# Optimization experiments

Measured on AMD Instinct MI355X. Metric: run time of the kernel, lower is better.

Reference implementation:

```python
import jax, jax.numpy as jnp
import numpy as np
import math

L, Bt, IN, H = 512, 128, 512, 60


def setup_inputs() -> dict:
    key = jax.random.key(0)
    k1, k2, k3 = jax.random.split(key, 3)
    inp = jax.random.normal(k1, (L, Bt, IN), dtype=jnp.float32)
    W = jax.random.normal(k2, (H, IN), dtype=jnp.float32) / np.sqrt(IN)
    b = jnp.zeros((H,), dtype=jnp.float32)
    alphabet = jax.random.uniform(k3, (H, 3), dtype=jnp.float32, minval=-math.pi, maxval=math.pi)
    bond_lengths = jnp.array([132.868, 145.801, 152.326], dtype=jnp.float32)
    bond_angles = jnp.array([2.028, 2.124, 1.941], dtype=jnp.float32)
    return {"inp": inp, "W": W, "b": b, "alphabet": alphabet,
            "bond_lengths": bond_lengths, "bond_angles": bond_angles}


def reference(inp, W, b, alphabet, bond_lengths, bond_angles):
    Lr, Bb = inp.shape[0], inp.shape[1]
    # mixture over alphabet of torsion angles
    x = jax.nn.softmax(inp @ W.T + b, axis=2)                 # (L, B, H)
    phi = jnp.arctan2(x @ jnp.sin(alphabet), x @ jnp.cos(alphabet))  # (L, B, 3)
    # per residue i the loop consumes phi[i].T -> bond index is fastest axis
    phi_f = phi.transpose(0, 2, 1).reshape(Lr * 3, Bb)        # (3L, B)
    r = jnp.tile(bond_lengths, Lr)[:, None]                   # (3L, 1)
    th = jnp.tile(bond_angles, Lr)[:, None]                   # (3L, 1)
    # SRF coordinates of every new atom
    c_tilde = jnp.stack([
        (r * jnp.cos(th)) * jnp.ones_like(phi_f),
        r * jnp.cos(phi_f) * jnp.sin(th),
        r * jnp.sin(phi_f) * jnp.sin(th),
    ], axis=-1)                                               # (3L, B, 3)

    e = jnp.eye(3, dtype=inp.dtype)
    carry0 = (jnp.broadcast_to(e[0], (Bb, 3)),
              jnp.broadcast_to(e[1], (Bb, 3)),
              jnp.broadcast_to(e[2], (Bb, 3)))

    def step(carry, ct):
        A, Bp, C = carry                                      # each (B, 3)
        BC = C - Bp
        bc = BC / jnp.linalg.norm(BC, axis=1, keepdims=True)
        AB = Bp - A
        Nv = jnp.cross(AB, bc)
        n = Nv / jnp.linalg.norm(Nv, axis=1, keepdims=True)
        # D = C + R @ c_tilde, R columns = [bc, n x bc, n]
        D = C + bc * ct[:, 0:1] + jnp.cross(n, bc) * ct[:, 1:2] + n * ct[:, 2:3]
        return (Bp, C, D), D

    _, coords = jax.lax.scan(step, carry0, c_tilde)           # (3L, B, 3)
    return coords
```

## Files before the change

### kernel.cpp

```cpp
#include <hip/hip_runtime.h>
#include <math.h>

#define LSEQ  512
#define BT    128
#define INF   512
#define HH    60
#define NSTEP 1536
#define CH2   6

#define MTILE 64
#define KSTG  128
#define BROW  136

typedef __attribute__((ext_vector_type(8))) short bf16x8;
typedef __attribute__((ext_vector_type(4))) float floatx4;
typedef __attribute__((ext_vector_type(4))) unsigned short ushortx4;

__device__ __forceinline__ unsigned short bf16_rn(float x) {
  unsigned u = __float_as_uint(x);
  return (unsigned short)((u + 0x7FFFu + ((u >> 16) & 1u)) >> 16);
}
__device__ __forceinline__ void split2(float x, unsigned short& h, unsigned short& l) {
  h = bf16_rn(x);
  float hf = __uint_as_float(((unsigned)h) << 16);
  l = bf16_rn(x - hf);
}

__global__ __launch_bounds__(256, 4) void k_phi(
    const float* __restrict__ inp, const float* __restrict__ W,
    const float* __restrict__ bias, const float* __restrict__ alphabet,
    float* __restrict__ phi_out) {
  __shared__ unsigned short BhL[64 * BROW];
  __shared__ unsigned short BlL[64 * BROW];
  __shared__ float sS[HH * 3], sC[HH * 3], sBias[64];

  const int tid  = threadIdx.x;
  const int lane = tid & 63;
  const int wid  = tid >> 6;
  const int c    = lane & 15;
  const int quad = lane >> 4;
  const int row0 = blockIdx.x * MTILE;

  if (tid < HH * 3) { float a = alphabet[tid]; sS[tid] = __sinf(a); sC[tid] = __cosf(a); }
  if (tid >= 192 && tid < 256) { int n = tid - 192; sBias[n] = (n < HH) ? bias[n] : 0.f; }

  floatx4 acc[4];
#pragma unroll
  for (int nt = 0; nt < 4; ++nt) acc[nt] = (floatx4){0.f, 0.f, 0.f, 0.f};

  const float* ap0 = inp + (size_t)(row0 + wid * 16 + c) * INF + quad * 8;

  float4 pa0 = *(const float4*)(ap0);
  float4 pa1 = *(const float4*)(ap0 + 4);

  for (int stg = 0; stg < 4; ++stg) {
    const int kbase = stg * KSTG;
    if (stg) __syncthreads();
#pragma unroll
    for (int i = 0; i < 8; ++i) {
      const int chunk = i * 256 + tid;
      const int r  = chunk >> 5;
      const int j4 = (chunk & 31) * 4;
      float4 wv = make_float4(0.f, 0.f, 0.f, 0.f);
      if (r < HH) wv = *(const float4*)(W + (size_t)r * INF + kbase + j4);
      ushortx4 hv, lv;
      unsigned short hb, lb;
      split2(wv.x, hb, lb); hv[0] = hb; lv[0] = lb;
      split2(wv.y, hb, lb); hv[1] = hb; lv[1] = lb;
      split2(wv.z, hb, lb); hv[2] = hb; lv[2] = lb;
      split2(wv.w, hb, lb); hv[3] = hb; lv[3] = lb;
      *(ushortx4*)&BhL[r * BROW + j4] = hv;
      *(ushortx4*)&BlL[r * BROW + j4] = lv;
    }
    __syncthreads();

#pragma unroll
    for (int ks = 0; ks < 4; ++ks) {
      const int kl = ks * 32;
      const int kg = kbase + kl;
      float4 a00 = pa0, a01 = pa1;
      if (kg + 32 < INF) {
        pa0 = *(const float4*)(ap0 + kg + 32);
        pa1 = *(const float4*)(ap0 + kg + 36);
      }
      bf16x8 Bh[4], Bl[4];
#pragma unroll
      for (int nt = 0; nt < 4; ++nt) {
        const int boff = (nt * 16 + c) * BROW + kl + quad * 8;
        Bh[nt] = *(const bf16x8*)&BhL[boff];
        Bl[nt] = *(const bf16x8*)&BlL[boff];
      }
      bf16x8 Ah, Al;
      {
        float av[8] = {a00.x,a00.y,a00.z,a00.w,a01.x,a01.y,a01.z,a01.w};
#pragma unroll
        for (int j = 0; j < 8; ++j) {
          unsigned short hb, lb; split2(av[j], hb, lb);
          Ah[j] = (short)hb; Al[j] = (short)lb;
        }
      }
#pragma unroll
      for (int nt = 0; nt < 4; ++nt) {
        acc[nt] = __builtin_amdgcn_mfma_f32_16x16x32_bf16(Ah, Bh[nt], acc[nt], 0, 0, 0);
        acc[nt] = __builtin_amdgcn_mfma_f32_16x16x32_bf16(Ah, Bl[nt], acc[nt], 0, 0, 0);
        acc[nt] = __builtin_amdgcn_mfma_f32_16x16x32_bf16(Al, Bh[nt], acc[nt], 0, 0, 0);
      }
    }
  }

#pragma unroll
  for (int reg = 0; reg < 4; ++reg) {
    float lg[4];  bool val[4];
#pragma unroll
    for (int nt = 0; nt < 4; ++nt) {
      const int n = nt * 16 + c;
      val[nt] = (n < HH);
      lg[nt] = acc[nt][reg] + sBias[n];
    }
    float m = -1e30f;
#pragma unroll
    for (int nt = 0; nt < 4; ++nt) if (val[nt]) m = fmaxf(m, lg[nt]);
#pragma unroll
    for (int d = 1; d < 16; d <<= 1) m = fmaxf(m, __shfl_xor(m, d, 64));

    float s0=0.f,c0=0.f,s1=0.f,c1=0.f,s2=0.f,c2=0.f;
#pragma unroll
    for (int nt = 0; nt < 4; ++nt) {
      const int n = nt * 16 + c;
      float e = val[nt] ? __expf(lg[nt] - m) : 0.f;
      s0 = fmaf(e, sS[n*3+0], s0);  c0 = fmaf(e, sC[n*3+0], c0);
      s1 = fmaf(e, sS[n*3+1], s1);  c1 = fmaf(e, sC[n*3+1], c1);
      s2 = fmaf(e, sS[n*3+2], s2);  c2 = fmaf(e, sC[n*3+2], c2);
    }
#pragma unroll
    for (int d = 1; d < 16; d <<= 1) {
      s0 += __shfl_xor(s0, d, 64);  c0 += __shfl_xor(c0, d, 64);
      s1 += __shfl_xor(s1, d, 64);  c1 += __shfl_xor(c1, d, 64);
      s2 += __shfl_xor(s2, d, 64);  c2 += __shfl_xor(c2, d, 64);
    }
    if (c == 0) {
      const int row = row0 + wid * 16 + quad * 4 + reg;
      const int l  = row >> 7;
      const int bb = row & 127;
      float* pp = phi_out + (size_t)bb * NSTEP + 3 * l;
      pp[0] = atan2f(s0, c0);
      pp[1] = atan2f(s1, c1);
      pp[2] = atan2f(s2, c2);
    }
  }
}

struct Xf { float r[9]; float p[3]; };

__device__ __forceinline__ Xf compose(const Xf& A, const Xf& B) {
  Xf o;
#pragma unroll
  for (int i = 0; i < 3; ++i) {
#pragma unroll
    for (int j = 0; j < 3; ++j) {
      o.r[i*3+j] = fmaf(A.r[i*3+0], B.r[0+j],
                   fmaf(A.r[i*3+1], B.r[3+j],
                        A.r[i*3+2] * B.r[6+j]));
    }
    o.p[i] = fmaf(A.r[i*3+0], B.p[0],
             fmaf(A.r[i*3+1], B.p[1],
             fmaf(A.r[i*3+2], B.p[2], A.p[i])));
  }
  return o;
}

__device__ __forceinline__ Xf make_T(float phi, float st, float ct, float r) {
  float sp = __sinf(phi), cp = __cosf(phi);
  Xf T;
  T.r[0] = ct;      T.r[1] = -st;     T.r[2] = 0.f;
  T.r[3] = cp * st; T.r[4] = ct * cp; T.r[5] = -sp;
  T.r[6] = sp * st; T.r[7] = ct * sp; T.r[8] = cp;
  T.p[0] = r * ct;  T.p[1] = r * T.r[3]; T.p[2] = r * T.r[6];
  return T;
}

__device__ __forceinline__ void set_identity(Xf& X) {
  X.r[0]=1.f; X.r[1]=0.f; X.r[2]=0.f;
  X.r[3]=0.f; X.r[4]=1.f; X.r[5]=0.f;
  X.r[6]=0.f; X.r[7]=0.f; X.r[8]=1.f;
  X.p[0]=0.f; X.p[1]=0.f; X.p[2]=0.f;
}

__global__ __launch_bounds__(256) void k_scan(
    const float* __restrict__ phi, const float* __restrict__ bl,
    const float* __restrict__ ba, float* __restrict__ out) {
  __shared__ Xf wt[4];

  const int b = blockIdx.x;
  const int t = threadIdx.x & 63;
  const int w = threadIdx.x >> 6;
  const int g = threadIdx.x;

  float st[3], ct[3], rr[3];
#pragma unroll
  for (int j = 0; j < 3; ++j) {
    float a = ba[j];
    st[j] = __sinf(a); ct[j] = __cosf(a); rr[j] = bl[j];
  }

  float f[CH2];
  const float2* ph2 = (const float2*)(phi + (size_t)b * NSTEP + g * CH2);
#pragma unroll
  for (int q = 0; q < CH2/2; ++q) {
    float2 v = ph2[q];
    f[2*q+0] = v.x; f[2*q+1] = v.y;
  }

  Xf Q = make_T(f[0], st[0], ct[0], rr[0]);
#pragma unroll
  for (int s = 1; s < CH2; ++s)
    Q = compose(Q, make_T(f[s], st[s%3], ct[s%3], rr[s%3]));

#pragma unroll
  for (int d = 1; d < 64; d <<= 1) {
    Xf O;
#pragma unroll
    for (int q = 0; q < 9; ++q) O.r[q] = __shfl_up(Q.r[q], d, 64);
#pragma unroll
    for (int q = 0; q < 3; ++q) O.p[q] = __shfl_up(Q.p[q], d, 64);
    if (t < d) set_identity(O);
    Q = compose(O, Q);
  }

  if (t == 63) wt[w] = Q;
  __syncthreads();

  Xf E;
#pragma unroll
  for (int q = 0; q < 9; ++q) E.r[q] = __shfl_up(Q.r[q], 1, 64);
#pragma unroll
  for (int q = 0; q < 3; ++q) E.p[q] = __shfl_up(Q.p[q], 1, 64);
  if (t == 0) set_identity(E);

  Xf S0;
  S0.r[0] = 0.f;                  S0.r[1] = 0.816496580927726f;   S0.r[2] = 0.5773502691896258f;
  S0.r[3] = -0.7071067811865475f; S0.r[4] = -0.4082482904638631f; S0.r[5] = 0.5773502691896258f;
  S0.r[6] = 0.7071067811865475f;  S0.r[7] = -0.4082482904638631f; S0.r[8] = 0.5773502691896258f;
  S0.p[0] = 0.f; S0.p[1] = 0.f; S0.p[2] = 1.f;

  Xf SP = S0;
#pragma unroll
  for (int i = 0; i < 3; ++i)
    if (i < w) SP = compose(SP, wt[i]);

  Xf cur = compose(SP, E);

  float* op = out + (size_t)(g * CH2) * (BT * 3) + b * 3;
#pragma unroll
  for (int s = 0; s < CH2; ++s) {
    cur = compose(cur, make_T(f[s], st[s%3], ct[s%3], rr[s%3]));
    op[(size_t)s * (BT*3) + 0] = cur.p[0];
    op[(size_t)s * (BT*3) + 1] = cur.p[1];
    op[(size_t)s * (BT*3) + 2] = cur.p[2];
  }
}

extern "C" void kernel_launch(void* const* d_in, const int* in_sizes, int n_in,
                              void* d_out, int out_size, void* d_ws, size_t ws_size,
                              hipStream_t stream) {
  const float* inp      = (const float*)d_in[0];
  const float* W        = (const float*)d_in[1];
  const float* bias     = (const float*)d_in[2];
  const float* alphabet = (const float*)d_in[3];
  const float* bl       = (const float*)d_in[4];
  const float* ba       = (const float*)d_in[5];
  float* out = (float*)d_out;

  float* phi = (float*)d_ws;

  k_phi<<<dim3((LSEQ*BT)/MTILE), dim3(256), 0, stream>>>(inp, W, bias, alphabet, phi);
  k_scan<<<dim3(BT), dim3(256), 0, stream>>>(phi, bl, ba, out);
}
```

Measured before the change: 221.3 us.

## Prefetch whole A stages ahead and use packed bf16 conversion in k_phi

Restructures the k_phi GEMM loop so each stage's full 128-wide A slice is loaded into registers one stage ahead (double-buffered A0/A1) while the current stage computes, replacing the previous one-step-ahead prefetch. The software bf16 rounding/split is replaced with the hardware v_cvt_pk_bf16_f32 instruction, which converts two floats per instruction. The launch-bounds occupancy hint drops from 4 to 3 waves to make room for the larger register footprint. The goal is to hide global load latency and cut VALU conversion work, at the cost of higher register pressure and lower occupancy.

```diff
diff --git a/kernel.cpp b/kernel.cpp
--- a/kernel.cpp
+++ b/kernel.cpp
@@ -14,19 +14,63 @@
 
 typedef __attribute__((ext_vector_type(8))) short bf16x8;
 typedef __attribute__((ext_vector_type(4))) float floatx4;
-typedef __attribute__((ext_vector_type(4))) unsigned short ushortx4;
-
-__device__ __forceinline__ unsigned short bf16_rn(float x) {
-  unsigned u = __float_as_uint(x);
-  return (unsigned short)((u + 0x7FFFu + ((u >> 16) & 1u)) >> 16);
-}
-__device__ __forceinline__ void split2(float x, unsigned short& h, unsigned short& l) {
-  h = bf16_rn(x);
-  float hf = __uint_as_float(((unsigned)h) << 16);
-  l = bf16_rn(x - hf);
-}
-
-__global__ __launch_bounds__(256, 4) void k_phi(
+
+__device__ __forceinline__ unsigned cvt_pk_bf16(float lo, float hi) {
+  unsigned r;
+  asm("v_cvt_pk_bf16_f32 %0, %1, %2" : "=v"(r) : "v"(lo), "v"(hi));
+  return r;
+}
+__device__ __forceinline__ void split_pair(float a0, float a1,
+                                           unsigned& hw, unsigned& lw) {
+  hw = cvt_pk_bf16(a0, a1);
+  float h0 = __uint_as_float(hw << 16);
+  float h1 = __uint_as_float(hw & 0xFFFF0000u);
+  lw = cvt_pk_bf16(a0 - h0, a1 - h1);
+}
+
+
+#define ISSUE_A(BUF, KB) \
+  { _Pragma("unroll") \
+    for (int ks_ = 0; ks_ < 4; ++ks_) { \
+      BUF[2*ks_]   = *(const float4*)(ap0 + (KB) + ks_*32); \
+      BUF[2*ks_+1] = *(const float4*)(ap0 + (KB) + ks_*32 + 4); } }
+
+#define STAGE_W(KB) \
+  { _Pragma("unroll") \
+    for (int i_ = 0; i_ < 8; ++i_) { \
+      const int chunk_ = i_ * 256 + tid; \
+      const int r_  = chunk_ >> 5; \
+      const int j4_ = (chunk_ & 31) * 4; \
+      float4 wv_ = make_float4(0.f, 0.f, 0.f, 0.f); \
+      if (r_ < HH) wv_ = *(const float4*)(W + (size_t)r_ * INF + (KB) + j4_); \
+      unsigned h01_, l01_, h23_, l23_; \
+      split_pair(wv_.x, wv_.y, h01_, l01_); \
+      split_pair(wv_.z, wv_.w, h23_, l23_); \
+      *(uint2*)&BhL[r_ * BROW + j4_] = make_uint2(h01_, h23_); \
+      *(uint2*)&BlL[r_ * BROW + j4_] = make_uint2(l01_, l23_); } }
+
+#define DO_STEPS(BUF) \
+  { _Pragma("unroll") \
+    for (int ks_ = 0; ks_ < 4; ++ks_) { \
+      const int kl_ = ks_ * 32; \
+      float4 x_ = BUF[2*ks_], y_ = BUF[2*ks_+1]; \
+      uint4 uh_, ul_; \
+      split_pair(x_.x, x_.y, uh_.x, ul_.x); \
+      split_pair(x_.z, x_.w, uh_.y, ul_.y); \
+      split_pair(y_.x, y_.y, uh_.z, ul_.z); \
+      split_pair(y_.z, y_.w, uh_.w, ul_.w); \
+      bf16x8 Ah_ = __builtin_bit_cast(bf16x8, uh_); \
+      bf16x8 Al_ = __builtin_bit_cast(bf16x8, ul_); \
+      _Pragma("unroll") \
+      for (int nt_ = 0; nt_ < 4; ++nt_) { \
+        const int boff_ = (nt_ * 16 + c) * BROW + kl_ + quad * 8; \
+        bf16x8 Bh_ = *(const bf16x8*)&BhL[boff_]; \
+        bf16x8 Bl_ = *(const bf16x8*)&BlL[boff_]; \
+        acc[nt_] = __builtin_amdgcn_mfma_f32_16x16x32_bf16(Ah_, Bh_, acc[nt_], 0, 0, 0); \
+        acc[nt_] = __builtin_amdgcn_mfma_f32_16x16x32_bf16(Ah_, Bl_, acc[nt_], 0, 0, 0); \
+        acc[nt_] = __builtin_amdgcn_mfma_f32_16x16x32_bf16(Al_, Bh_, acc[nt_], 0, 0, 0); } } }
+
+__global__ __launch_bounds__(256, 3) void k_phi(
     const float* __restrict__ inp, const float* __restrict__ W,
     const float* __restrict__ bias, const float* __restrict__ alphabet,
     float* __restrict__ phi_out) {
@@ -50,63 +94,27 @@
 
   const float* ap0 = inp + (size_t)(row0 + wid * 16 + c) * INF + quad * 8;
 
-  float4 pa0 = *(const float4*)(ap0);
-  float4 pa1 = *(const float4*)(ap0 + 4);
-
-  for (int stg = 0; stg < 4; ++stg) {
-    const int kbase = stg * KSTG;
-    if (stg) __syncthreads();
-#pragma unroll
-    for (int i = 0; i < 8; ++i) {
-      const int chunk = i * 256 + tid;
-      const int r  = chunk >> 5;
-      const int j4 = (chunk & 31) * 4;
-      float4 wv = make_float4(0.f, 0.f, 0.f, 0.f);
-      if (r < HH) wv = *(const float4*)(W + (size_t)r * INF + kbase + j4);
-      ushortx4 hv, lv;
-      unsigned short hb, lb;
-      split2(wv.x, hb, lb); hv[0] = hb; lv[0] = lb;
-      split2(wv.y, hb, lb); hv[1] = hb; lv[1] = lb;
-      split2(wv.z, hb, lb); hv[2] = hb; lv[2] = lb;
-      split2(wv.w, hb, lb); hv[3] = hb; lv[3] = lb;
-      *(ushortx4*)&BhL[r * BROW + j4] = hv;
-      *(ushortx4*)&BlL[r * BROW + j4] = lv;
-    }
-    __syncthreads();
-
-#pragma unroll
-    for (int ks = 0; ks < 4; ++ks) {
-      const int kl = ks * 32;
-      const int kg = kbase + kl;
-      float4 a00 = pa0, a01 = pa1;
-      if (kg + 32 < INF) {
-        pa0 = *(const float4*)(ap0 + kg + 32);
-        pa1 = *(const float4*)(ap0 + kg + 36);
-      }
-      bf16x8 Bh[4], Bl[4];
-#pragma unroll
-      for (int nt = 0; nt < 4; ++nt) {
-        const int boff = (nt * 16 + c) * BROW + kl + quad * 8;
-        Bh[nt] = *(const bf16x8*)&BhL[boff];
-        Bl[nt] = *(const bf16x8*)&BlL[boff];
-      }
-      bf16x8 Ah, Al;
-      {
-        float av[8] = {a00.x,a00.y,a00.z,a00.w,a01.x,a01.y,a01.z,a01.w};
-#pragma unroll
-        for (int j = 0; j < 8; ++j) {
-          unsigned short hb, lb; split2(av[j], hb, lb);
-          Ah[j] = (short)hb; Al[j] = (short)lb;
-        }
-      }
-#pragma unroll
-      for (int nt = 0; nt < 4; ++nt) {
-        acc[nt] = __builtin_amdgcn_mfma_f32_16x16x32_bf16(Ah, Bh[nt], acc[nt], 0, 0, 0);
-        acc[nt] = __builtin_amdgcn_mfma_f32_16x16x32_bf16(Ah, Bl[nt], acc[nt], 0, 0, 0);
-        acc[nt] = __builtin_amdgcn_mfma_f32_16x16x32_bf16(Al, Bh[nt], acc[nt], 0, 0, 0);
-      }
-    }
-  }
+  float4 A0[8], A1[8];
+
+  ISSUE_A(A0, 0);
+  STAGE_W(0);
+  __syncthreads();
+  ISSUE_A(A1, KSTG);
+  DO_STEPS(A0);
+  __syncthreads();
+  STAGE_W(KSTG);
+  __syncthreads();
+  ISSUE_A(A0, 2 * KSTG);
+  DO_STEPS(A1);
+  __syncthreads();
+  STAGE_W(2 * KSTG);
+  __syncthreads();
+  ISSUE_A(A1, 3 * KSTG);
+  DO_STEPS(A0);
+  __syncthreads();
+  STAGE_W(3 * KSTG);
+  __syncthreads();
+  DO_STEPS(A1);
 
 #pragma unroll
   for (int reg = 0; reg < 4; ++reg) {
```

New measurement: 228.3 us. 1.03x slower.

## Stage full W once per block with larger row tiles and deep A prefetch

Applied to the files above, without the earlier changes.

k_phi now uses 512-thread blocks covering 256 rows each, and converts the whole 60x512 W matrix into bf16 hi/lo split in LDS once per block instead of in four K stages with barriers. That cuts the number of times W is re-split from 1024 blocks to 256. The A operand is streamed with inline-asm global_load_dwordx4 through a 5-slot register ring using explicit vmcnt waits. Hardware packed bf16 conversion (v_cvt_pk_bf16_f32) replaces the manual rounding. The trade-off is much larger LDS use (about 134KB per block), more registers per thread and only 256 blocks in flight, which may limit occupancy.

```diff
diff --git a/kernel.cpp b/kernel.cpp
--- a/kernel.cpp
+++ b/kernel.cpp
@@ -8,30 +8,38 @@
 #define NSTEP 1536
 #define CH2   6
 
-#define MTILE 64
-#define KSTG  128
-#define BROW  136
+#define SROW  522
 
 typedef __attribute__((ext_vector_type(8))) short bf16x8;
 typedef __attribute__((ext_vector_type(4))) float floatx4;
-typedef __attribute__((ext_vector_type(4))) unsigned short ushortx4;
-
-__device__ __forceinline__ unsigned short bf16_rn(float x) {
-  unsigned u = __float_as_uint(x);
-  return (unsigned short)((u + 0x7FFFu + ((u >> 16) & 1u)) >> 16);
-}
-__device__ __forceinline__ void split2(float x, unsigned short& h, unsigned short& l) {
-  h = bf16_rn(x);
-  float hf = __uint_as_float(((unsigned)h) << 16);
-  l = bf16_rn(x - hf);
-}
-
-__global__ __launch_bounds__(256, 4) void k_phi(
+
+__device__ __forceinline__ unsigned cvt_pk_bf16(float lo, float hi) {
+  unsigned r;
+  asm("v_cvt_pk_bf16_f32 %0, %1, %2" : "=v"(r) : "v"(lo), "v"(hi));
+  return r;
+}
+__device__ __forceinline__ void split_pair(float a0, float a1,
+                                           unsigned& hw, unsigned& lw) {
+  hw = cvt_pk_bf16(a0, a1);
+  float h0 = __uint_as_float(hw << 16);
+  float h1 = __uint_as_float(hw & 0xFFFF0000u);
+  lw = cvt_pk_bf16(a0 - h0, a1 - h1);
+}
+
+#define GLOAD(dst, ptr, voff) \
+  asm volatile("global_load_dwordx4 %0, %1, %2" \
+               : "=v"(dst) : "v"(voff), "s"(ptr))
+
+#define WAIT_VM(n) \
+  do { asm volatile("s_waitcnt vmcnt(" #n ")" ::: "memory"); \
+       __builtin_amdgcn_sched_barrier(0); } while (0)
+
+__global__ __launch_bounds__(512, 2) void k_phi(
     const float* __restrict__ inp, const float* __restrict__ W,
     const float* __restrict__ bias, const float* __restrict__ alphabet,
     float* __restrict__ phi_out) {
-  __shared__ unsigned short BhL[64 * BROW];
-  __shared__ unsigned short BlL[64 * BROW];
+  __shared__ unsigned short BhL[64 * SROW];
+  __shared__ unsigned short BlL[64 * SROW];
   __shared__ float sS[HH * 3], sC[HH * 3], sBias[64];
 
   const int tid  = threadIdx.x;
@@ -39,113 +47,142 @@
   const int wid  = tid >> 6;
   const int c    = lane & 15;
   const int quad = lane >> 4;
-  const int row0 = blockIdx.x * MTILE;
+  const int row0 = blockIdx.x * 256;
 
   if (tid < HH * 3) { float a = alphabet[tid]; sS[tid] = __sinf(a); sC[tid] = __cosf(a); }
   if (tid >= 192 && tid < 256) { int n = tid - 192; sBias[n] = (n < HH) ? bias[n] : 0.f; }
 
-  floatx4 acc[4];
-#pragma unroll
-  for (int nt = 0; nt < 4; ++nt) acc[nt] = (floatx4){0.f, 0.f, 0.f, 0.f};
-
-  const float* ap0 = inp + (size_t)(row0 + wid * 16 + c) * INF + quad * 8;
-
-  float4 pa0 = *(const float4*)(ap0);
-  float4 pa1 = *(const float4*)(ap0 + 4);
-
-  for (int stg = 0; stg < 4; ++stg) {
-    const int kbase = stg * KSTG;
-    if (stg) __syncthreads();
+  {
+    const unsigned voffW = ((unsigned)(tid >> 7) * INF + (tid & 127) * 4) * 4u;
+    floatx4 Wb[15];
+#pragma unroll
+    for (int i = 0; i < 15; ++i)
+      GLOAD(Wb[i], W + (size_t)i * 4 * INF, voffW);
+    const int rb = tid >> 7;
+    const int j4 = (tid & 127) * 4;
+    WAIT_VM(7);
 #pragma unroll
     for (int i = 0; i < 8; ++i) {
-      const int chunk = i * 256 + tid;
-      const int r  = chunk >> 5;
-      const int j4 = (chunk & 31) * 4;
-      float4 wv = make_float4(0.f, 0.f, 0.f, 0.f);
-      if (r < HH) wv = *(const float4*)(W + (size_t)r * INF + kbase + j4);
-      ushortx4 hv, lv;
-      unsigned short hb, lb;
-      split2(wv.x, hb, lb); hv[0] = hb; lv[0] = lb;
-      split2(wv.y, hb, lb); hv[1] = hb; lv[1] = lb;
-      split2(wv.z, hb, lb); hv[2] = hb; lv[2] = lb;
-      split2(wv.w, hb, lb); hv[3] = hb; lv[3] = lb;
-      *(ushortx4*)&BhL[r * BROW + j4] = hv;
-      *(ushortx4*)&BlL[r * BROW + j4] = lv;
-    }
-    __syncthreads();
-
-#pragma unroll
-    for (int ks = 0; ks < 4; ++ks) {
-      const int kl = ks * 32;
-      const int kg = kbase + kl;
-      float4 a00 = pa0, a01 = pa1;
-      if (kg + 32 < INF) {
-        pa0 = *(const float4*)(ap0 + kg + 32);
-        pa1 = *(const float4*)(ap0 + kg + 36);
+      unsigned h01, l01, h23, l23;
+      split_pair(Wb[i][0], Wb[i][1], h01, l01);
+      split_pair(Wb[i][2], Wb[i][3], h23, l23);
+      const int r = i * 4 + rb;
+      *(uint2*)&BhL[r * SROW + j4] = make_uint2(h01, h23);
+      *(uint2*)&BlL[r * SROW + j4] = make_uint2(l01, l23);
+    }
+    WAIT_VM(0);
+#pragma unroll
+    for (int i = 8; i < 15; ++i) {
+      unsigned h01, l01, h23, l23;
+      split_pair(Wb[i][0], Wb[i][1], h01, l01);
+      split_pair(Wb[i][2], Wb[i][3], h23, l23);
+      const int r = i * 4 + rb;
+      *(uint2*)&BhL[r * SROW + j4] = make_uint2(h01, h23);
+      *(uint2*)&BlL[r * SROW + j4] = make_uint2(l01, l23);
+    }
+    for (int z = tid; z < 4 * SROW; z += 512) {
+      BhL[60 * SROW + z] = 0;
+      BlL[60 * SROW + z] = 0;
+    }
+  }
+  __syncthreads();
+
+  floatx4 acc[2][4];
+#pragma unroll
+  for (int g = 0; g < 2; ++g)
+#pragma unroll
+    for (int nt = 0; nt < 4; ++nt) acc[g][nt] = (floatx4){0.f, 0.f, 0.f, 0.f};
+
+  const float* aBase = inp + (size_t)row0 * INF;
+  unsigned voffA[2];
+#pragma unroll
+  for (int g = 0; g < 2; ++g)
+    voffA[g] = ((unsigned)(wid * 32 + g * 16 + c) * INF + quad * 8) * 4u;
+
+  floatx4 PF[5][2];
+
+#pragma unroll
+  for (int j = 0; j < 4; ++j) {
+    const int g = j >> 4, ks = j & 15;
+    GLOAD(PF[j % 5][0], aBase + ks * 32,     voffA[g]);
+    GLOAD(PF[j % 5][1], aBase + ks * 32 + 4, voffA[g]);
+  }
+
+#pragma unroll
+  for (int i = 0; i < 32; ++i) {
+    if (i + 4 < 32) {
+      const int j = i + 4, g = j >> 4, ks = j & 15;
+      GLOAD(PF[j % 5][0], aBase + ks * 32,     voffA[g]);
+      GLOAD(PF[j % 5][1], aBase + ks * 32 + 4, voffA[g]);
+    }
+    if (i < 28)       WAIT_VM(8);
+    else if (i == 28) WAIT_VM(6);
+    else if (i == 29) WAIT_VM(4);
+    else if (i == 30) WAIT_VM(2);
+    else              WAIT_VM(0);
+
+    const int g  = i >> 4;
+    const int ks = i & 15;
+    floatx4 x = PF[i % 5][0], y = PF[i % 5][1];
+    uint4 uh, ul;
+    split_pair(x[0], x[1], uh.x, ul.x);
+    split_pair(x[2], x[3], uh.y, ul.y);
+    split_pair(y[0], y[1], uh.z, ul.z);
+    split_pair(y[2], y[3], uh.w, ul.w);
+    bf16x8 Ah = __builtin_bit_cast(bf16x8, uh);
+    bf16x8 Al = __builtin_bit_cast(bf16x8, ul);
+#pragma unroll
+    for (int nt = 0; nt < 4; ++nt) {
+      const int boff = (nt * 16 + c) * SROW + ks * 32 + quad * 8;
+      bf16x8 Bh = *(const bf16x8*)&BhL[boff];
+      bf16x8 Bl = *(const bf16x8*)&BlL[boff];
+      acc[g][nt] = __builtin_amdgcn_mfma_f32_16x16x32_bf16(Ah, Bh, acc[g][nt], 0, 0, 0);
+      acc[g][nt] = __builtin_amdgcn_mfma_f32_16x16x32_bf16(Ah, Bl, acc[g][nt], 0, 0, 0);
+      acc[g][nt] = __builtin_amdgcn_mfma_f32_16x16x32_bf16(Al, Bh, acc[g][nt], 0, 0, 0);
+    }
+  }
+
+#pragma unroll
+  for (int g = 0; g < 2; ++g) {
+#pragma unroll
+    for (int reg = 0; reg < 4; ++reg) {
+      float lg[4];  bool val[4];
+#pragma unroll
+      for (int nt = 0; nt < 4; ++nt) {
+        const int n = nt * 16 + c;
+        val[nt] = (n < HH);
+        lg[nt] = acc[g][nt][reg] + sBias[n];
       }
-      bf16x8 Bh[4], Bl[4];
+      float m = -1e30f;
+#pragma unroll
+      for (int nt = 0; nt < 4; ++nt) if (val[nt]) m = fmaxf(m, lg[nt]);
+#pragma unroll
+      for (int d = 1; d < 16; d <<= 1) m = fmaxf(m, __shfl_xor(m, d, 64));
+
+      float s0=0.f,c0=0.f,s1=0.f,c1=0.f,s2=0.f,c2=0.f;
 #pragma unroll
       for (int nt = 0; nt < 4; ++nt) {
-        const int boff = (nt * 16 + c) * BROW + kl + quad * 8;
-        Bh[nt] = *(const bf16x8*)&BhL[boff];
-        Bl[nt] = *(const bf16x8*)&BlL[boff];
+        const int n = nt * 16 + c;
+        float e = val[nt] ? __expf(lg[nt] - m) : 0.f;
+        s0 = fmaf(e, sS[n*3+0], s0);  c0 = fmaf(e, sC[n*3+0], c0);
+        s1 = fmaf(e, sS[n*3+1], s1);  c1 = fmaf(e, sC[n*3+1], c1);
+        s2 = fmaf(e, sS[n*3+2], s2);  c2 = fmaf(e, sC[n*3+2], c2);
       }
-      bf16x8 Ah, Al;
-      {
-        float av[8] = {a00.x,a00.y,a00.z,a00.w,a01.x,a01.y,a01.z,a01.w};
-#pragma unroll
-        for (int j = 0; j < 8; ++j) {
-          unsigned short hb, lb; split2(av[j], hb, lb);
-          Ah[j] = (short)hb; Al[j] = (short)lb;
-        }
+#pragma unroll
+      for (int d = 1; d < 16; d <<= 1) {
+        s0 += __shfl_xor(s0, d, 64);  c0 += __shfl_xor(c0, d, 64);
+        s1 += __shfl_xor(s1, d, 64);  c1 += __shfl_xor(c1, d, 64);
+        s2 += __shfl_xor(s2, d, 64);  c2 += __shfl_xor(c2, d, 64);
       }
-#pragma unroll
-      for (int nt = 0; nt < 4; ++nt) {
-        acc[nt] = __builtin_amdgcn_mfma_f32_16x16x32_bf16(Ah, Bh[nt], acc[nt], 0, 0, 0);
-        acc[nt] = __builtin_amdgcn_mfma_f32_16x16x32_bf16(Ah, Bl[nt], acc[nt], 0, 0, 0);
-        acc[nt] = __builtin_amdgcn_mfma_f32_16x16x32_bf16(Al, Bh[nt], acc[nt], 0, 0, 0);
+      if (c == 0) {
+        const int row = row0 + wid * 32 + g * 16 + quad * 4 + reg;
+        const int l  = row >> 7;
+        const int bb = row & 127;
+        float* pp = phi_out + (size_t)bb * NSTEP + 3 * l;
+        pp[0] = atan2f(s0, c0);
+        pp[1] = atan2f(s1, c1);
+        pp[2] = atan2f(s2, c2);
       }
-    }
-  }
-
-#pragma unroll
-  for (int reg = 0; reg < 4; ++reg) {
-    float lg[4];  bool val[4];
-#pragma unroll
-    for (int nt = 0; nt < 4; ++nt) {
-      const int n = nt * 16 + c;
-      val[nt] = (n < HH);
-      lg[nt] = acc[nt][reg] + sBias[n];
-    }
-    float m = -1e30f;
-#pragma unroll
-    for (int nt = 0; nt < 4; ++nt) if (val[nt]) m = fmaxf(m, lg[nt]);
-#pragma unroll
-    for (int d = 1; d < 16; d <<= 1) m = fmaxf(m, __shfl_xor(m, d, 64));
-
-    float s0=0.f,c0=0.f,s1=0.f,c1=0.f,s2=0.f,c2=0.f;
-#pragma unroll
-    for (int nt = 0; nt < 4; ++nt) {
-      const int n = nt * 16 + c;
-      float e = val[nt] ? __expf(lg[nt] - m) : 0.f;
-      s0 = fmaf(e, sS[n*3+0], s0);  c0 = fmaf(e, sC[n*3+0], c0);
-      s1 = fmaf(e, sS[n*3+1], s1);  c1 = fmaf(e, sC[n*3+1], c1);
-      s2 = fmaf(e, sS[n*3+2], s2);  c2 = fmaf(e, sC[n*3+2], c2);
-    }
-#pragma unroll
-    for (int d = 1; d < 16; d <<= 1) {
-      s0 += __shfl_xor(s0, d, 64);  c0 += __shfl_xor(c0, d, 64);
-      s1 += __shfl_xor(s1, d, 64);  c1 += __shfl_xor(c1, d, 64);
-      s2 += __shfl_xor(s2, d, 64);  c2 += __shfl_xor(c2, d, 64);
-    }
-    if (c == 0) {
-      const int row = row0 + wid * 16 + quad * 4 + reg;
-      const int l  = row >> 7;
-      const int bb = row & 127;
-      float* pp = phi_out + (size_t)bb * NSTEP + 3 * l;
-      pp[0] = atan2f(s0, c0);
-      pp[1] = atan2f(s1, c1);
-      pp[2] = atan2f(s2, c2);
     }
   }
 }
@@ -273,6 +310,6 @@
 
   float* phi = (float*)d_ws;
 
-  k_phi<<<dim3((LSEQ*BT)/MTILE), dim3(256), 0, stream>>>(inp, W, bias, alphabet, phi);
+  k_phi<<<dim3(256), dim3(512), 0, stream>>>(inp, W, bias, alphabet, phi);
   k_scan<<<dim3(BT), dim3(256), 0, stream>>>(phi, bl, ba, out);
 }
```

Measured after the change: 221.1 us. No clear change (-0.1%).
